# Kernel optimization log

Measured on AMD Instinct MI355X. Metric: run time of the kernel, lower is better.

The kernel has to match this reference:

```python
import jax, jax.numpy as jnp
import numpy as np

N = 100000
C_IN = 256
C_OUT = 256
LN_EPS = 1e-5


def setup_inputs() -> dict:
    key = jax.random.key(0)
    ks = jax.random.split(key, 6)
    x = jax.random.normal(ks[0], (N, C_IN), dtype=jnp.float32)
    idx1 = jax.random.randint(ks[1], (N,), 0, N, dtype=jnp.int64 if jax.config.jax_enable_x64 else jnp.int32)
    idx2 = jax.random.randint(ks[2], (N,), 0, N, dtype=idx1.dtype)
    idx3 = jax.random.randint(ks[3], (N,), 0, N, dtype=idx1.dtype)
    idx4 = jax.random.randint(ks[4], (N,), 0, N, dtype=idx1.dtype)
    W = jax.random.normal(ks[5], (5 * C_IN, C_OUT), dtype=jnp.float32) * (1.0 / np.sqrt(5 * C_IN))
    b = jnp.zeros((C_OUT,), dtype=jnp.float32)
    gamma = jnp.ones((C_OUT,), dtype=jnp.float32)
    beta = jnp.zeros((C_OUT,), dtype=jnp.float32)
    return {"x": x, "idx1": idx1, "idx2": idx2, "idx3": idx3, "idx4": idx4,
            "W": W, "b": b, "gamma": gamma, "beta": beta}


def reference(x, idx1, idx2, idx3, idx4, W, b, gamma, beta):
    # Four sparse-mm neighbor gathers (one nonzero of value 1 per row)
    a = x[idx1]
    bb = x[idx2]
    c = x[idx3]
    d = x[idx4]
    # symmetric combine + concat -> [N, 5*C_IN]
    patch = jnp.concatenate([x, jnp.abs(a - c), a + c, jnp.abs(bb - d), bb + d], axis=-1)
    y = patch @ W + b
    # LayerNorm over channels
    mu = jnp.mean(y, axis=-1, keepdims=True)
    var = jnp.mean(jnp.square(y - mu), axis=-1, keepdims=True)
    y = (y - mu) * jax.lax.rsqrt(var + LN_EPS) * gamma + beta
    # residual (in_channels == out_channels -> identity projection)
    y = y + x
    # torch nn.GELU default is exact (erf) gelu
    return jax.nn.gelu(y, approximate=False)
```

## Files before the change

### kernel.cpp

```cpp
#include <hip/hip_runtime.h>


#define N_ROWS   100000
#define C        256
#define BK       32
#define NCHUNK   40
#define BM       64
#define CHUNK_V  1024
#define LN_EPS   1e-5f

typedef __bf16 bf16;
typedef bf16  bf16x8 __attribute__((ext_vector_type(8)));
typedef float f32x4  __attribute__((ext_vector_type(4)));

union BV  { bf16x8 v; bf16 h[8]; };
union FV2 { float4 q[2]; float f[8]; };

__device__ __forceinline__ void lds_barrier() {
    __builtin_amdgcn_sched_barrier(0);
    asm volatile("s_waitcnt lgkmcnt(0)");
    __builtin_amdgcn_s_barrier();
    __builtin_amdgcn_sched_barrier(0);
}

__global__ void wprep(const float* __restrict__ W, bf16* __restrict__ Wt) {
    int t = blockIdx.x * 256 + threadIdx.x;
    if (t >= NCHUNK * 4 * 4 * 64) return;
    int lane = t & 63;
    int ni   = (t >> 6) & 3;
    int wv   = (t >> 8) & 3;
    int kc   = t >> 10;
    int l16  = lane & 15, quad = lane >> 4;
    int n = wv * 64 + ni * 16 + l16;
    int base;
    if (kc < 8)       base = kc * 32;
    else if (kc < 24) { int u = kc - 8;  base = 256 + (u & 1) * 256 + (u >> 1) * 32; }
    else              { int u = kc - 24; base = 768 + (u & 1) * 256 + (u >> 1) * 32; }
    BV o;
    #pragma unroll
    for (int e = 0; e < 8; ++e) {
        int kRow = base + quad * 8 + e;
        o.h[e] = (bf16)W[(size_t)kRow * C + n];
    }
    ((bf16x8*)Wt)[t] = o.v;
}

__global__ __launch_bounds__(256, 3)
void fused(const float* __restrict__ x,
           const int* __restrict__ idx1, const int* __restrict__ idx2,
           const int* __restrict__ idx3, const int* __restrict__ idx4,
           const bf16* __restrict__ Wt,
           const float* __restrict__ bias,
           const float* __restrict__ gamma_, const float* __restrict__ beta_,
           float* __restrict__ out)
{
    __shared__ __align__(16) union {
        bf16 a[2][BM * BK];
        struct { float rsum[BM][4]; float rsq[BM][4]; float mu[BM]; float rs[BM]; } red;
    } SA;

    const int tid  = threadIdx.x;
    const int lane = tid & 63;
    const int wv   = tid >> 6;
    const int quad = lane >> 4;
    const int l16  = lane & 15;
    const int r0   = blockIdx.x * BM;

    const int r_st = tid >> 2;
    const int q_st = tid & 3;
    int gr_self = r0 + r_st; if (gr_self >= N_ROWS) gr_self = 0;
    const int ia = idx1[gr_self], ib = idx2[gr_self];
    const int ic = idx3[gr_self], id = idx4[gr_self];
    const float* xself = x + (size_t)gr_self * C + (q_st << 3);

    const int a_w_off = r_st * 32 + ((q_st ^ ((r_st >> 1) & 3)) << 3);
    int a_r_off[4];
    #pragma unroll
    for (int mi = 0; mi < 4; ++mi) {
        int m = mi * 16 + l16;
        a_r_off[mi] = m * 32 + ((quad ^ ((m >> 1) & 3)) << 3);
    }

    const bf16x8* Wq = (const bf16x8*)Wt + wv * 256 + lane;

    f32x4 acc[4][4] = {};
    bf16x8 hold;
    bf16x8 wf[4], wfn[4];
    FV2 cur_a, cur_c;
    FV2 nxt_a, nxt_c;
    int cur_mode, nxt_mode;

    {
        const float4* p0 = (const float4*)xself;
        float4 s0 = p0[0], s1 = p0[1];
        const float4* p1 = (const float4*)(xself + 32);
        cur_a.q[0] = p1[0]; cur_a.q[1] = p1[1]; cur_mode = 1;
        #pragma unroll
        for (int j = 0; j < 4; ++j) wf[j] = Wq[j * 64];
        FV2 u; u.q[0] = s0; u.q[1] = s1;
        BV b0;
        #pragma unroll
        for (int j = 0; j < 8; ++j) b0.h[j] = (bf16)u.f[j];
        *(bf16x8*)&SA.a[0][a_w_off] = b0.v;
    }
    lds_barrier();

    #pragma unroll
    for (int kc = 0; kc < NCHUNK; ++kc) {
        const int kn = kc + 1;
        const int kp = kc + 2;

        nxt_mode = 0;
        if (kp < NCHUNK) {
            if (kp < 8) {
                nxt_mode = 1;
                const float4* p = (const float4*)(xself + (kp << 5));
                nxt_a.q[0] = p[0]; nxt_a.q[1] = p[1];
            } else {
                int u = (kp < 24) ? (kp - 8) : (kp - 24);
                if (!(u & 1)) {
                    nxt_mode = 2;
                    int rA = (kp < 24) ? ia : ib;
                    int rC = (kp < 24) ? ic : id;
                    int off = ((u >> 1) << 5) + (q_st << 3);
                    const float4* pa = (const float4*)(x + (size_t)rA * C + off);
                    const float4* pc = (const float4*)(x + (size_t)rC * C + off);
                    nxt_a.q[0] = pa[0]; nxt_a.q[1] = pa[1];
                    nxt_c.q[0] = pc[0]; nxt_c.q[1] = pc[1];
                }
            }
        }

        if (kn < NCHUNK) {
            const bf16x8* wp = Wq + (size_t)kn * CHUNK_V;
            #pragma unroll
            for (int j = 0; j < 4; ++j) wfn[j] = wp[j * 64];
        }

        if (kn < NCHUNK) {
            BV sv;
            if (cur_mode == 1) {
                #pragma unroll
                for (int j = 0; j < 8; ++j) sv.h[j] = (bf16)cur_a.f[j];
            } else if (cur_mode == 2) {
                BV hs;
                #pragma unroll
                for (int j = 0; j < 8; ++j) {
                    sv.h[j] = (bf16)fabsf(cur_a.f[j] - cur_c.f[j]);
                    hs.h[j] = (bf16)(cur_a.f[j] + cur_c.f[j]);
                }
                hold = hs.v;
            } else {
                sv.v = hold;
            }
            *(bf16x8*)&SA.a[kn & 1][a_w_off] = sv.v;
        }

        {
            const bf16* Ab = SA.a[kc & 1];
            bf16x8 af[4];
            #pragma unroll
            for (int mi = 0; mi < 4; ++mi)
                af[mi] = *(const bf16x8*)&Ab[a_r_off[mi]];
            __builtin_amdgcn_s_setprio(1);
            #pragma unroll
            for (int mi = 0; mi < 4; ++mi)
                #pragma unroll
                for (int ni = 0; ni < 4; ++ni)
                    acc[mi][ni] = __builtin_amdgcn_mfma_f32_16x16x32_bf16(
                        af[mi], wf[ni], acc[mi][ni], 0, 0, 0);
            __builtin_amdgcn_s_setprio(0);
        }

        if (kn < NCHUNK) {
            #pragma unroll
            for (int j = 0; j < 4; ++j) wf[j] = wfn[j];
        }
        cur_a = nxt_a; cur_c = nxt_c; cur_mode = nxt_mode;

        if (kn < NCHUNK) lds_barrier();
    }

    float bcol[4], gcol[4], ecol[4];
    #pragma unroll
    for (int ni = 0; ni < 4; ++ni) {
        int cidx = wv * 64 + ni * 16 + l16;
        bcol[ni] = bias[cidx]; gcol[ni] = gamma_[cidx]; ecol[ni] = beta_[cidx];
    }
    #pragma unroll
    for (int mi = 0; mi < 4; ++mi)
        #pragma unroll
        for (int ni = 0; ni < 4; ++ni)
            #pragma unroll
            for (int rg = 0; rg < 4; ++rg)
                acc[mi][ni][rg] += bcol[ni];

    #pragma unroll
    for (int mi = 0; mi < 4; ++mi) {
        #pragma unroll
        for (int rg = 0; rg < 4; ++rg) {
            float s = 0.f, q = 0.f;
            #pragma unroll
            for (int ni = 0; ni < 4; ++ni) {
                float y = acc[mi][ni][rg];
                s += y; q += y * y;
            }
            #pragma unroll
            for (int m = 1; m <= 8; m <<= 1) {
                s += __shfl_xor(s, m, 64);
                q += __shfl_xor(q, m, 64);
            }
            if (l16 == 0) {
                int row = mi * 16 + quad * 4 + rg;
                SA.red.rsum[row][wv] = s;
                SA.red.rsq [row][wv] = q;
            }
        }
    }
    __syncthreads();
    if (tid < BM) {
        float s  = SA.red.rsum[tid][0] + SA.red.rsum[tid][1] + SA.red.rsum[tid][2] + SA.red.rsum[tid][3];
        float q  = SA.red.rsq [tid][0] + SA.red.rsq [tid][1] + SA.red.rsq [tid][2] + SA.red.rsq [tid][3];
        float mu = s * (1.0f / C);
        float var = q * (1.0f / C) - mu * mu;
        SA.red.mu[tid] = mu;
        SA.red.rs[tid] = rsqrtf(var + LN_EPS);
    }
    __syncthreads();

    #pragma unroll
    for (int mi = 0; mi < 4; ++mi) {
        #pragma unroll
        for (int rg = 0; rg < 4; ++rg) {
            int row  = mi * 16 + quad * 4 + rg;
            int grow = r0 + row;
            if (grow >= N_ROWS) continue;
            float mu = SA.red.mu[row], rs = SA.red.rs[row];
            #pragma unroll
            for (int ni = 0; ni < 4; ++ni) {
                int cidx = wv * 64 + ni * 16 + l16;
                float y = (acc[mi][ni][rg] - mu) * rs * gcol[ni] + ecol[ni];
                y += x[(size_t)grow * C + cidx];
                float g = 0.5f * y * (1.0f + erff(y * 0.70710678118654752f));
                out[(size_t)grow * C + cidx] = g;
            }
        }
    }
}

extern "C" void kernel_launch(void* const* d_in, const int* in_sizes, int n_in,
                              void* d_out, int out_size, void* d_ws, size_t ws_size,
                              hipStream_t stream) {
    const float* x  = (const float*)d_in[0];
    const int*   i1 = (const int*)d_in[1];
    const int*   i2 = (const int*)d_in[2];
    const int*   i3 = (const int*)d_in[3];
    const int*   i4 = (const int*)d_in[4];
    const float* W  = (const float*)d_in[5];
    const float* b  = (const float*)d_in[6];
    const float* gm = (const float*)d_in[7];
    const float* bt = (const float*)d_in[8];
    float* outp = (float*)d_out;
    bf16* Wt = (bf16*)d_ws;

    wprep<<<(NCHUNK * 4 * 4 * 64 + 255) / 256, 256, 0, stream>>>(W, Wt);
    fused<<<(N_ROWS + BM - 1) / BM, 256, 0, stream>>>(
        x, i1, i2, i3, i4, Wt, b, gm, bt, outp);
}
```

Before: 336.5 us.

## Process two K-chunks per iteration to halve barriers and remove mode branching

Restructures the main K loop so each iteration stages and consumes two 32-wide K chunks (double-sized LDS buffers), halving the number of block barriers. The gather mode logic is simplified: each pair either converts two self chunks or computes |a-c| and a+c from one gathered pair, removing the held-register and mode variables. W fragments are now loaded at the top of the same iteration instead of being prefetched one chunk ahead, which may expose global load latency before the MFMAs.

New measurement: 339.9 us. About the same (+1.0%).

```diff
diff --git a/kernel.cpp b/kernel.cpp
--- a/kernel.cpp
+++ b/kernel.cpp
@@ -5,6 +5,7 @@
 #define C        256
 #define BK       32
 #define NCHUNK   40
+#define NITER    20
 #define BM       64
 #define CHUNK_V  1024
 #define LN_EPS   1e-5f
@@ -55,7 +56,7 @@
            float* __restrict__ out)
 {
     __shared__ __align__(16) union {
-        bf16 a[2][BM * BK];
+        bf16 a[2][2][BM * BK];
         struct { float rsum[BM][4]; float rsq[BM][4]; float mu[BM]; float rs[BM]; } red;
     } SA;
 
@@ -84,84 +85,83 @@
     const bf16x8* Wq = (const bf16x8*)Wt + wv * 256 + lane;
 
     f32x4 acc[4][4] = {};
-    bf16x8 hold;
-    bf16x8 wf[4], wfn[4];
-    FV2 cur_a, cur_c;
-    FV2 nxt_a, nxt_c;
-    int cur_mode, nxt_mode;
+    bf16x8 wf[8];
+    FV2 cA, cB;
+    FV2 nA, nB;
 
     {
         const float4* p0 = (const float4*)xself;
-        float4 s0 = p0[0], s1 = p0[1];
         const float4* p1 = (const float4*)(xself + 32);
-        cur_a.q[0] = p1[0]; cur_a.q[1] = p1[1]; cur_mode = 1;
-        #pragma unroll
-        for (int j = 0; j < 4; ++j) wf[j] = Wq[j * 64];
-        FV2 u; u.q[0] = s0; u.q[1] = s1;
-        BV b0;
-        #pragma unroll
-        for (int j = 0; j < 8; ++j) b0.h[j] = (bf16)u.f[j];
-        *(bf16x8*)&SA.a[0][a_w_off] = b0.v;
+        FV2 u0, u1;
+        u0.q[0] = p0[0]; u0.q[1] = p0[1];
+        u1.q[0] = p1[0]; u1.q[1] = p1[1];
+        const float4* p2 = (const float4*)(xself + 64);
+        const float4* p3 = (const float4*)(xself + 96);
+        cA.q[0] = p2[0]; cA.q[1] = p2[1];
+        cB.q[0] = p3[0]; cB.q[1] = p3[1];
+        BV b0, b1;
+        #pragma unroll
+        for (int j = 0; j < 8; ++j) { b0.h[j] = (bf16)u0.f[j]; b1.h[j] = (bf16)u1.f[j]; }
+        *(bf16x8*)&SA.a[0][0][a_w_off] = b0.v;
+        *(bf16x8*)&SA.a[0][1][a_w_off] = b1.v;
     }
     lds_barrier();
 
     #pragma unroll
-    for (int kc = 0; kc < NCHUNK; ++kc) {
-        const int kn = kc + 1;
-        const int kp = kc + 2;
-
-        nxt_mode = 0;
-        if (kp < NCHUNK) {
-            if (kp < 8) {
-                nxt_mode = 1;
-                const float4* p = (const float4*)(xself + (kp << 5));
-                nxt_a.q[0] = p[0]; nxt_a.q[1] = p[1];
+    for (int i = 0; i < NITER; ++i) {
+        {
+            const bf16x8* w0 = Wq + (size_t)(2 * i)     * CHUNK_V;
+            const bf16x8* w1 = Wq + (size_t)(2 * i + 1) * CHUNK_V;
+            #pragma unroll
+            for (int j = 0; j < 4; ++j) { wf[j] = w0[j * 64]; wf[4 + j] = w1[j * 64]; }
+        }
+
+        const int jp = i + 2;
+        if (jp < NITER) {
+            if (jp < 4) {
+                const float4* pa = (const float4*)(xself + ((2 * jp)     << 5));
+                const float4* pb = (const float4*)(xself + ((2 * jp + 1) << 5));
+                nA.q[0] = pa[0]; nA.q[1] = pa[1];
+                nB.q[0] = pb[0]; nB.q[1] = pb[1];
             } else {
-                int u = (kp < 24) ? (kp - 8) : (kp - 24);
-                if (!(u & 1)) {
-                    nxt_mode = 2;
-                    int rA = (kp < 24) ? ia : ib;
-                    int rC = (kp < 24) ? ic : id;
-                    int off = ((u >> 1) << 5) + (q_st << 3);
-                    const float4* pa = (const float4*)(x + (size_t)rA * C + off);
-                    const float4* pc = (const float4*)(x + (size_t)rC * C + off);
-                    nxt_a.q[0] = pa[0]; nxt_a.q[1] = pa[1];
-                    nxt_c.q[0] = pc[0]; nxt_c.q[1] = pc[1];
+                const int p   = (jp < 12) ? (jp - 4) : (jp - 12);
+                const int rA  = (jp < 12) ? ia : ib;
+                const int rC  = (jp < 12) ? ic : id;
+                const int off = (p << 5) + (q_st << 3);
+                const float4* pa = (const float4*)(x + (size_t)rA * C + off);
+                const float4* pc = (const float4*)(x + (size_t)rC * C + off);
+                nA.q[0] = pa[0]; nA.q[1] = pa[1];
+                nB.q[0] = pc[0]; nB.q[1] = pc[1];
+            }
+        }
+
+        const int jn = i + 1;
+        if (jn < NITER) {
+            BV s0, s1;
+            if (jn < 4) {
+                #pragma unroll
+                for (int j = 0; j < 8; ++j) {
+                    s0.h[j] = (bf16)cA.f[j];
+                    s1.h[j] = (bf16)cB.f[j];
                 }
-            }
-        }
-
-        if (kn < NCHUNK) {
-            const bf16x8* wp = Wq + (size_t)kn * CHUNK_V;
-            #pragma unroll
-            for (int j = 0; j < 4; ++j) wfn[j] = wp[j * 64];
-        }
-
-        if (kn < NCHUNK) {
-            BV sv;
-            if (cur_mode == 1) {
-                #pragma unroll
-                for (int j = 0; j < 8; ++j) sv.h[j] = (bf16)cur_a.f[j];
-            } else if (cur_mode == 2) {
-                BV hs;
+            } else {
                 #pragma unroll
                 for (int j = 0; j < 8; ++j) {
-                    sv.h[j] = (bf16)fabsf(cur_a.f[j] - cur_c.f[j]);
-                    hs.h[j] = (bf16)(cur_a.f[j] + cur_c.f[j]);
+                    s0.h[j] = (bf16)fabsf(cA.f[j] - cB.f[j]);
+                    s1.h[j] = (bf16)(cA.f[j] + cB.f[j]);
                 }
-                hold = hs.v;
-            } else {
-                sv.v = hold;
-            }
-            *(bf16x8*)&SA.a[kn & 1][a_w_off] = sv.v;
+            }
+            *(bf16x8*)&SA.a[jn & 1][0][a_w_off] = s0.v;
+            *(bf16x8*)&SA.a[jn & 1][1][a_w_off] = s1.v;
         }
 
         {
-            const bf16* Ab = SA.a[kc & 1];
+            const bf16* Ab0 = SA.a[i & 1][0];
+            const bf16* Ab1 = SA.a[i & 1][1];
             bf16x8 af[4];
             #pragma unroll
             for (int mi = 0; mi < 4; ++mi)
-                af[mi] = *(const bf16x8*)&Ab[a_r_off[mi]];
+                af[mi] = *(const bf16x8*)&Ab0[a_r_off[mi]];
             __builtin_amdgcn_s_setprio(1);
             #pragma unroll
             for (int mi = 0; mi < 4; ++mi)
@@ -170,15 +170,21 @@
                     acc[mi][ni] = __builtin_amdgcn_mfma_f32_16x16x32_bf16(
                         af[mi], wf[ni], acc[mi][ni], 0, 0, 0);
             __builtin_amdgcn_s_setprio(0);
-        }
-
-        if (kn < NCHUNK) {
-            #pragma unroll
-            for (int j = 0; j < 4; ++j) wf[j] = wfn[j];
-        }
-        cur_a = nxt_a; cur_c = nxt_c; cur_mode = nxt_mode;
-
-        if (kn < NCHUNK) lds_barrier();
+            #pragma unroll
+            for (int mi = 0; mi < 4; ++mi)
+                af[mi] = *(const bf16x8*)&Ab1[a_r_off[mi]];
+            __builtin_amdgcn_s_setprio(1);
+            #pragma unroll
+            for (int mi = 0; mi < 4; ++mi)
+                #pragma unroll
+                for (int ni = 0; ni < 4; ++ni)
+                    acc[mi][ni] = __builtin_amdgcn_mfma_f32_16x16x32_bf16(
+                        af[mi], wf[4 + ni], acc[mi][ni], 0, 0, 0);
+            __builtin_amdgcn_s_setprio(0);
+        }
+
+        cA = nA; cB = nB;
+        if (i < NITER - 1) lds_barrier();
     }
 
     float bcol[4], gcol[4], ecol[4];
```
